# Kernel tuning notes

Hardware: AMD Instinct MI355X
Metric: run time of the kernel (lower is better)

Reference implementation:

```python
import jax, jax.numpy as jnp
import numpy as np

B, CTX = 16, 64
H, W = 1024, 1024
EPS = 1e-12
STD = 0.001


def setup_inputs() -> dict:
    key = jax.random.key(0)
    ks = jax.random.split(key, 6)
    x = jax.random.normal(ks[0], (B, CTX), dtype=jnp.float32)
    # context_transform_input / gate: Linear(CTX -> 12) with bias
    lim = 1.0 / np.sqrt(CTX)
    W_in = jax.random.uniform(ks[1], (12, CTX), jnp.float32, -lim, lim)
    b_in = jax.random.uniform(ks[2], (12,), jnp.float32, -lim, lim)
    W_gate = jax.random.uniform(ks[3], (12, CTX), jnp.float32, -lim, lim)
    b_gate = jax.random.uniform(ks[4], (12,), jnp.float32, -lim, lim)
    # base weights: [1, 2, 2, H, W, 2], normal(0, STD)
    weights = STD * jax.random.normal(ks[5], (1, 2, 2, H, W, 2), dtype=jnp.float32)
    return {"x": x, "W_in": W_in, "b_in": b_in, "W_gate": W_gate,
            "b_gate": b_gate, "weights": weights}


def _clerp(z1, z2, c):
    # complex lerp: z1 + c*(z2 - z1) with complex c packed in last dim
    c0, c1 = c[..., 0], c[..., 1]
    re = (1 - c0) * z1[..., 0] + c0 * z2[..., 0] - c1 * (z2[..., 1] - z1[..., 1])
    im = (1 - c0) * z1[..., 1] + c0 * z2[..., 1] + c1 * (z2[..., 0] - z1[..., 0])
    return jnp.stack([re, im], axis=-1)


def _caddmul(z1, z2, bias):
    # bias + z1*z2 (complex), packed in last dim
    re = bias[..., 0] + (z1[..., 0] * z2[..., 0] - z1[..., 1] * z2[..., 1])
    im = bias[..., 1] + (z1[..., 0] * z2[..., 1] + z1[..., 1] * z2[..., 0])
    return jnp.stack([re, im], axis=-1)


def reference(x, W_in, b_in, W_gate, b_gate, weights):
    b = x.shape[0]
    x_t = x @ W_in.T + b_in          # [B, 12]
    x_g = x @ W_gate.T + b_gate      # [B, 12]
    mod = (x_t * jnp.tanh(x_g)).reshape(b, 3, 2, 1, 1, 2)  # broadcasts over H, W
    shift_lerp = jnp.array([0.5, 0.0], dtype=x.dtype)
    shift_scale = jnp.array([1.0, 0.0], dtype=x.dtype)
    param_l = mod[:, 0] + shift_lerp   # [B, 2, 1, 1, 2]
    param_b = mod[:, 1]
    param_s = mod[:, 2] + shift_scale
    w0, w1 = weights[:, 0], weights[:, 1]   # [1, 2, H, W, 2] each
    z = _clerp(w0, w1, param_l)             # [B, 2, H, W, 2]
    z = _caddmul(z, param_s, param_b)       # [B, 2, H, W, 2]
    denom = jnp.sqrt(jnp.sum(z[:, 1] ** 2, axis=-1) + EPS)[..., None]  # [B, H, W, 1]
    theta = z[:, 1] / denom
    return jnp.sum(z[:, 0] * theta, axis=-1)  # [B, H, W]
```

## Files before the change

### kernel.cpp

```cpp
#include <hip/hip_runtime.h>
#include <math.h>

#define HW (1024*1024)
#define BATCH 16

__global__ __launch_bounds__(192) void params_kernel(
    const float* __restrict__ x,
    const float* __restrict__ W_in,
    const float* __restrict__ b_in,
    const float* __restrict__ W_gate,
    const float* __restrict__ b_gate,
    float* __restrict__ par)
{
    __shared__ float smod[BATCH][12];
    int t = threadIdx.x;
    int b = t / 12, j = t % 12;
    if (b < BATCH) {
        float xt = b_in[j], xg = b_gate[j];
        for (int k = 0; k < 64; ++k) {
            float xv = x[b * 64 + k];
            xt = fmaf(xv, W_in[j * 64 + k], xt);
            xg = fmaf(xv, W_gate[j * 64 + k], xg);
        }
        smod[b][j] = xt * tanhf(xg);
    }
    __syncthreads();
    if (t < 32) {
        int bb = t >> 1, c = t & 1;
        float l0 = smod[bb][0 * 4 + c * 2 + 0] + 0.5f;
        float l1 = smod[bb][0 * 4 + c * 2 + 1];
        float br = smod[bb][1 * 4 + c * 2 + 0];
        float bi = smod[bb][1 * 4 + c * 2 + 1];
        float s0 = smod[bb][2 * 4 + c * 2 + 0] + 1.0f;
        float s1 = smod[bb][2 * 4 + c * 2 + 1];
        float omr = 1.0f - l0, omi = -l1;
        float Ar = s0 * omr - s1 * omi;
        float Ai = s0 * omi + s1 * omr;
        float Br = s0 * l0 - s1 * l1;
        float Bi = s0 * l1 + s1 * l0;
        float* p = par + (bb * 2 + c) * 6;
        p[0] = Ar; p[1] = Ai; p[2] = Br; p[3] = Bi; p[4] = br; p[5] = bi;
    }
}

__global__ __launch_bounds__(256) void main_kernel(
    const float* __restrict__ wts,
    const float* __restrict__ par,
    float* __restrict__ out)
{
    __shared__ float sp[192];
    int t = threadIdx.x;
    if (t < 192) sp[t] = par[t];
    __syncthreads();

    int idx = blockIdx.x * 256 + t;
    const float4* w4 = (const float4*)wts;

    float4 Wv[4][2];
#pragma unroll
    for (int jc = 0; jc < 4; ++jc) {
        Wv[jc][0] = w4[jc * (HW / 2) + idx * 2 + 0];
        Wv[jc][1] = w4[jc * (HW / 2) + idx * 2 + 1];
    }
    const float* w00 = (const float*)Wv[0];
    const float* w01 = (const float*)Wv[1];
    const float* w10 = (const float*)Wv[2];
    const float* w11 = (const float*)Wv[3];

    float4* out4 = (float4*)out;
#pragma unroll
    for (int b = 0; b < BATCH; ++b) {
        const float* p0 = &sp[(b * 2 + 0) * 6];
        const float* p1 = &sp[(b * 2 + 1) * 6];
        float A0r = p0[0], A0i = p0[1], B0r = p0[2], B0i = p0[3], c0r = p0[4], c0i = p0[5];
        float A1r = p1[0], A1i = p1[1], B1r = p1[2], B1i = p1[3], c1r = p1[4], c1i = p1[5];
        float4 o;
        float* op = (float*)&o;
#pragma unroll
        for (int p = 0; p < 4; ++p) {
            float a0r = w00[p * 2], a0i = w00[p * 2 + 1];
            float b0r = w10[p * 2], b0i = w10[p * 2 + 1];
            float a1r = w01[p * 2], a1i = w01[p * 2 + 1];
            float b1r = w11[p * 2], b1i = w11[p * 2 + 1];
            float z0r = c0r + A0r * a0r - A0i * a0i + B0r * b0r - B0i * b0i;
            float z0i = c0i + A0r * a0i + A0i * a0r + B0r * b0i + B0i * b0r;
            float z1r = c1r + A1r * a1r - A1i * a1i + B1r * b1r - B1i * b1i;
            float z1i = c1i + A1r * a1i + A1i * a1r + B1r * b1i + B1i * b1r;
            float rs = rsqrtf(z1r * z1r + z1i * z1i + 1e-12f);
            op[p] = (z0r * z1r + z0i * z1i) * rs;
        }
        out4[b * (HW / 4) + idx] = o;
    }
}

extern "C" void kernel_launch(void* const* d_in, const int* in_sizes, int n_in,
                              void* d_out, int out_size, void* d_ws, size_t ws_size,
                              hipStream_t stream) {
    const float* x      = (const float*)d_in[0];
    const float* W_in   = (const float*)d_in[1];
    const float* b_in   = (const float*)d_in[2];
    const float* W_gate = (const float*)d_in[3];
    const float* b_gate = (const float*)d_in[4];
    const float* wts    = (const float*)d_in[5];
    float* out = (float*)d_out;
    float* par = (float*)d_ws;

    params_kernel<<<1, 192, 0, stream>>>(x, W_in, b_in, W_gate, b_gate, par);
    main_kernel<<<1024, 256, 0, stream>>>(wts, par, out);
}
```

Before: 29.06 us.

## Fuse parameter computation into main kernel and use nontemporal output stores

Merges the single-block parameter kernel into the main streaming kernel, so each block recomputes the small 16x12 linear+tanh projection into shared memory instead of going through a workspace and a second launch. The dot products now use float4 loads, and the output stores become nontemporal vector stores. This removes one launch and the serialization between the two kernels, at the cost of redundant per-block compute and reads of x and the weight matrices (which should hit cache).

```diff
diff --git a/kernel.cpp b/kernel.cpp
--- a/kernel.cpp
+++ b/kernel.cpp
@@ -4,23 +4,34 @@
 #define HW (1024*1024)
 #define BATCH 16
 
-__global__ __launch_bounds__(192) void params_kernel(
+typedef float fx4 __attribute__((ext_vector_type(4)));
+
+__global__ __launch_bounds__(256) void fused_kernel(
     const float* __restrict__ x,
     const float* __restrict__ W_in,
     const float* __restrict__ b_in,
     const float* __restrict__ W_gate,
     const float* __restrict__ b_gate,
-    float* __restrict__ par)
+    const float* __restrict__ wts,
+    float* __restrict__ out)
 {
     __shared__ float smod[BATCH][12];
+    __shared__ float sp[192];
     int t = threadIdx.x;
-    int b = t / 12, j = t % 12;
-    if (b < BATCH) {
+
+    if (t < 192) {
+        int b = t / 12, j = t % 12;
+        const float4* x4  = (const float4*)(x + b * 64);
+        const float4* wi4 = (const float4*)(W_in + j * 64);
+        const float4* wg4 = (const float4*)(W_gate + j * 64);
         float xt = b_in[j], xg = b_gate[j];
-        for (int k = 0; k < 64; ++k) {
-            float xv = x[b * 64 + k];
-            xt = fmaf(xv, W_in[j * 64 + k], xt);
-            xg = fmaf(xv, W_gate[j * 64 + k], xg);
+#pragma unroll
+        for (int k = 0; k < 16; ++k) {
+            float4 xv = x4[k], wi = wi4[k], wg = wg4[k];
+            xt = fmaf(xv.x, wi.x, xt); xg = fmaf(xv.x, wg.x, xg);
+            xt = fmaf(xv.y, wi.y, xt); xg = fmaf(xv.y, wg.y, xg);
+            xt = fmaf(xv.z, wi.z, xt); xg = fmaf(xv.z, wg.z, xg);
+            xt = fmaf(xv.w, wi.w, xt); xg = fmaf(xv.w, wg.w, xg);
         }
         smod[b][j] = xt * tanhf(xg);
     }
@@ -38,19 +49,9 @@
         float Ai = s0 * omi + s1 * omr;
         float Br = s0 * l0 - s1 * l1;
         float Bi = s0 * l1 + s1 * l0;
-        float* p = par + (bb * 2 + c) * 6;
+        float* p = sp + (bb * 2 + c) * 6;
         p[0] = Ar; p[1] = Ai; p[2] = Br; p[3] = Bi; p[4] = br; p[5] = bi;
     }
-}
-
-__global__ __launch_bounds__(256) void main_kernel(
-    const float* __restrict__ wts,
-    const float* __restrict__ par,
-    float* __restrict__ out)
-{
-    __shared__ float sp[192];
-    int t = threadIdx.x;
-    if (t < 192) sp[t] = par[t];
     __syncthreads();
 
     int idx = blockIdx.x * 256 + t;
@@ -67,15 +68,14 @@
     const float* w10 = (const float*)Wv[2];
     const float* w11 = (const float*)Wv[3];
 
-    float4* out4 = (float4*)out;
+    fx4* out4 = (fx4*)out;
 #pragma unroll
     for (int b = 0; b < BATCH; ++b) {
         const float* p0 = &sp[(b * 2 + 0) * 6];
         const float* p1 = &sp[(b * 2 + 1) * 6];
         float A0r = p0[0], A0i = p0[1], B0r = p0[2], B0i = p0[3], c0r = p0[4], c0i = p0[5];
         float A1r = p1[0], A1i = p1[1], B1r = p1[2], B1i = p1[3], c1r = p1[4], c1i = p1[5];
-        float4 o;
-        float* op = (float*)&o;
+        fx4 o;
 #pragma unroll
         for (int p = 0; p < 4; ++p) {
             float a0r = w00[p * 2], a0i = w00[p * 2 + 1];
@@ -87,9 +87,9 @@
             float z1r = c1r + A1r * a1r - A1i * a1i + B1r * b1r - B1i * b1i;
             float z1i = c1i + A1r * a1i + A1i * a1r + B1r * b1i + B1i * b1r;
             float rs = rsqrtf(z1r * z1r + z1i * z1i + 1e-12f);
-            op[p] = (z0r * z1r + z0i * z1i) * rs;
+            o[p] = (z0r * z1r + z0i * z1i) * rs;
         }
-        out4[b * (HW / 4) + idx] = o;
+        __builtin_nontemporal_store(o, &out4[b * (HW / 4) + idx]);
     }
 }
 
@@ -103,8 +103,6 @@
     const float* b_gate = (const float*)d_in[4];
     const float* wts    = (const float*)d_in[5];
     float* out = (float*)d_out;
-    float* par = (float*)d_ws;
 
-    params_kernel<<<1, 192, 0, stream>>>(x, W_in, b_in, W_gate, b_gate, par);
-    main_kernel<<<1024, 256, 0, stream>>>(wts, par, out);
+    fused_kernel<<<1024, 256, 0, stream>>>(x, W_in, b_in, W_gate, b_gate, wts, out);
 }
```

Measured after the change: 32.73 us. 12.6% more time.
